# Kernel optimization log

Measured on AMD Instinct MI355X. Metric: run time of the kernel, lower is better.

Reference implementation:

```python
import jax, jax.numpy as jnp
import numpy as np

HEADS = 4

def _pair_msg(H, w2, B, xsrc):
    # H:[E,mid] radial-MLP hidden; w2:[mid,co,ci,nf]; B:[E,m_out,m_in,nf] CG/SH basis; xsrc:[E,ci,m_in]
    tmp = jnp.einsum('epqf,eiq->eipf', B, xsrc)          # basis-weighted input  [E,ci,m_out,nf]
    R = jnp.einsum('eh,hoif->eoif', H, w2)               # per-edge radial weights [E,co,ci,nf]
    return jnp.einsum('eoif,eipf->eop', R, tmp)          # edge message [E,co,m_out]

def _conv_edges(ef, w1, w2_nf1, w2_11, b00, b01, b10, b11, x0s, x1s):
    # pair index p = 2*d_in + d_out; pairs (0,0),(0,1),(1,0) have nf=1, pair (1,1) has nf=3
    H = jax.nn.relu(jnp.einsum('ef,pfh->peh', ef, w1))
    m0 = _pair_msg(H[0], w2_nf1[0][..., None], b00, x0s) + _pair_msg(H[2], w2_nf1[2][..., None], b10, x1s)
    m1 = _pair_msg(H[1], w2_nf1[1][..., None], b01, x0s) + _pair_msg(H[3], w2_11, b11, x1s)
    return m0, m1

def _seg_softmax(z, dst, n):
    m = jax.ops.segment_max(z, dst, num_segments=n)
    m = jnp.where(jnp.isfinite(m), m, 0.0)
    e = jnp.exp(z - m[dst])
    s = jax.ops.segment_sum(e, dst, num_segments=n)
    return e / (s[dst] + 1e-9)

def _norm_se3(x, g, b, eps=1e-3):
    n = jnp.sqrt((x * x).sum(-1) + 1e-12)                # per-channel irrep norm [N,C]
    mu = n.mean(-1, keepdims=True)
    var = ((n - mu) ** 2).mean(-1, keepdims=True)
    ln = (n - mu) / jnp.sqrt(var + 1e-5) * g + b
    return x * (jax.nn.relu(ln) / (n + eps))[..., None]

def _forward(x0, x1, edge_feat, b00, b01, b10, b11, kv_w1, kv_w2_nf1, kv_w2_11,
             wq, wproj, norm_gamma, norm_beta, fc_w1, fc_w2_nf1, fc_w2_11, fc_wself,
             edge_src, edge_dst):
    N = x0.shape[0]
    E = edge_src.shape[0]
    L = kv_w1.shape[0]
    ckv = wq.shape[-1]
    scale = 1.0 / np.sqrt((ckv // HEADS) * 4)            # key feats per head over degrees 0,1 (1+3 comps)
    hs = lambda t: t.reshape(t.shape[0], HEADS, ckv // HEADS, t.shape[-1])
    for l in range(L):
        # AttentionBlockSE3: ConvSE3 -> per-edge key/value; LinearSE3 -> query; seg-softmax attention
        kv0, kv1 = _conv_edges(edge_feat, kv_w1[l], kv_w2_nf1[l], kv_w2_11[l],
                               b00, b01, b10, b11, x0[edge_src], x1[edge_src])
        k0, v0 = kv0[:, :ckv], kv0[:, ckv:]
        k1, v1 = kv1[:, :ckv], kv1[:, ckv:]
        q0 = jnp.einsum('ncm,cd->ndm', x0, wq[l, 0])
        q1 = jnp.einsum('ncm,cd->ndm', x1, wq[l, 1])
        z = (hs(q0)[edge_dst] * hs(k0)).sum((2, 3)) + (hs(q1)[edge_dst] * hs(k1)).sum((2, 3))
        alpha = _seg_softmax(z * scale, edge_dst, N)     # [E,heads]
        a0 = (alpha[:, :, None, None] * hs(v0)).reshape(E, ckv, 1)
        a1 = (alpha[:, :, None, None] * hs(v1)).reshape(E, ckv, 3)
        o0 = jax.ops.segment_sum(a0, edge_dst, num_segments=N)
        o1 = jax.ops.segment_sum(a1, edge_dst, num_segments=N)
        # project concat(attn_out, skip) per degree, then NormSE3
        x0 = jnp.einsum('ncm,cd->ndm', jnp.concatenate([o0, x0], 1), wproj[l, 0])
        x1 = jnp.einsum('ncm,cd->ndm', jnp.concatenate([o1, x1], 1), wproj[l, 1])
        x0 = _norm_se3(x0, norm_gamma[l, 0], norm_beta[l, 0])
        x1 = _norm_se3(x1, norm_gamma[l, 1], norm_beta[l, 1])
    # final ConvSE3 with self-interaction, scatter-aggregated over dst nodes
    m0, m1 = _conv_edges(edge_feat, fc_w1, fc_w2_nf1, fc_w2_11,
                         b00, b01, b10, b11, x0[edge_src], x1[edge_src])
    y0 = jax.ops.segment_sum(m0, edge_dst, num_segments=N) + jnp.einsum('ncm,cd->ndm', x0, fc_wself[0])
    y1 = jax.ops.segment_sum(m1, edge_dst, num_segments=N) + jnp.einsum('ncm,cd->ndm', x1, fc_wself[1])
    return jnp.concatenate([y0.reshape(N, -1), y1.reshape(N, -1)], axis=1)

def setup_inputs() -> dict:
    key = jax.random.key(0)
    ks = jax.random.split(key, 20)
    N, E, C, L = 8192, 131072, 16, 2
    Fe, mid, KV, ckv, Co = 16, 16, 16, 8, 8
    f = lambda k, s, sc=1.0: jax.random.normal(k, s, dtype=jnp.float32) * sc
    return {
        'x0': f(ks[0], (N, C, 1)),
        'x1': f(ks[1], (N, C, 3)),
        'edge_feat': f(ks[2], (E, Fe)),
        'b00': f(ks[3], (E, 1, 1, 1)),
        'b01': f(ks[4], (E, 3, 1, 1)),
        'b10': f(ks[5], (E, 1, 3, 1)),
        'b11': f(ks[6], (E, 3, 3, 3)),
        'kv_w1': f(ks[7], (L, 4, Fe, mid), 0.1),
        'kv_w2_nf1': f(ks[8], (L, 3, mid, KV, C), 0.1),
        'kv_w2_11': f(ks[9], (L, mid, KV, C, 3), 0.1),
        'wq': f(ks[10], (L, 2, C, ckv), 0.1),
        'wproj': f(ks[11], (L, 2, ckv + C, C), 0.1),
        'norm_gamma': jnp.ones((L, 2, C), dtype=jnp.float32),
        'norm_beta': jnp.zeros((L, 2, C), dtype=jnp.float32),
        'fc_w1': f(ks[12], (4, Fe, mid), 0.1),
        'fc_w2_nf1': f(ks[13], (3, mid, Co, C), 0.1),
        'fc_w2_11': f(ks[14], (mid, Co, C, 3), 0.1),
        'fc_wself': f(ks[15], (2, C, Co), 0.1),
        'edge_src': jax.random.randint(ks[16], (E,), 0, N, dtype=jnp.int32),
        'edge_dst': jax.random.randint(ks[17], (E,), 0, N, dtype=jnp.int32),
    }

def reference(x0, x1, edge_feat, b00, b01, b10, b11, kv_w1, kv_w2_nf1, kv_w2_11,
              wq, wproj, norm_gamma, norm_beta, fc_w1, fc_w2_nf1, fc_w2_11, fc_wself,
              edge_src, edge_dst):
    return _forward(x0, x1, edge_feat, b00, b01, b10, b11, kv_w1, kv_w2_nf1, kv_w2_11,
                    wq, wproj, norm_gamma, norm_beta, fc_w1, fc_w2_nf1, fc_w2_11, fc_wself,
                    edge_src, edge_dst)
```

## Files before the change

kernel.cpp:

```cpp
#include <hip/hip_runtime.h>
#include <hip/hip_fp16.h>
#include <math.h>


typedef _Float16 half8 __attribute__((ext_vector_type(8)));
typedef float f32x4 __attribute__((ext_vector_type(4)));

union AF {
    half8 h8;
    __half2 h2[4];
};
union U32h2 {
    unsigned u;
    __half2 h;
};

__global__ void k_hist(const int* __restrict__ dst, int* __restrict__ counts, int E) {
    int e = blockIdx.x * 256 + threadIdx.x;
    if (e < E) atomicAdd(&counts[dst[e]], 1);
}

__global__ __launch_bounds__(1024) void k_scan(const int* __restrict__ counts,
                                               int* __restrict__ rowptr,
                                               int* __restrict__ cursor,
                                               int N, int CH) {
    __shared__ int part[1024];
    int t = threadIdx.x;
    int s = 0;
    for (int i = 0; i < CH; ++i) {
        int idx = t * CH + i;
        if (idx < N) s += counts[idx];
    }
    part[t] = s;
    __syncthreads();
    for (int off = 1; off < 1024; off <<= 1) {
        int v = (t >= off) ? part[t - off] : 0;
        __syncthreads();
        part[t] += v;
        __syncthreads();
    }
    int run = (t == 0) ? 0 : part[t - 1];
    for (int i = 0; i < CH; ++i) {
        int idx = t * CH + i;
        if (idx < N) {
            rowptr[idx] = run;
            cursor[idx] = run;
            run += counts[idx];
        }
    }
    if (t == 0) rowptr[N] = part[1023];
}

__global__ void k_scatter(const int* __restrict__ dst, int* __restrict__ cursor,
                          int* __restrict__ pose, int E) {
    int e = blockIdx.x * 256 + threadIdx.x;
    if (e < E) {
        int pos = atomicAdd(&cursor[dst[e]], 1);
        pose[e] = pos;
    }
}

__global__ void k_misc(const float* __restrict__ x0, const float* __restrict__ x1,
                       const float* __restrict__ ef,
                       float* __restrict__ xs0, float* __restrict__ xs1,
                       unsigned short* __restrict__ efh, int n0, int n1, int n2) {
    int i = blockIdx.x * 256 + threadIdx.x;
    if (i < n0) { xs0[i] = x0[i]; return; }
    i -= n0;
    if (i < n1) { xs1[i] = x1[i]; return; }
    i -= n1;
    if (i < n2) efh[i] = __half_as_ushort(__float2half(ef[i]));
}

__global__ void k_prepw(const float* __restrict__ kvw1, const float* __restrict__ fcw1,
                        const float* __restrict__ kvw2n, const float* __restrict__ kvw211,
                        const float* __restrict__ fcw2n, const float* __restrict__ fcw211,
                        unsigned short* __restrict__ Wfrag) {
    int t = blockIdx.x * 256 + threadIdx.x;
    if (t >= 156 * 64 * 8) return;
    int j = t & 7;
    int lane = (t >> 3) & 63;
    int row = t >> 9;
    int quad = lane >> 4, m = lane & 15;
    int c = row / 52, r = row % 52;
    int KVO = (c < 2) ? 16 : 8;
    const float* w1src = (c < 2) ? (kvw1 + c * 1024) : fcw1;
    const float* w2n = (c < 2) ? (kvw2n + c * 12288) : fcw2n;
    const float* w211 = (c < 2) ? (kvw211 + c * 12288) : fcw211;
    float v = 0.f;
    if (r < 4) {
        if (quad < 2) v = w1src[r * 256 + (quad * 8 + j) * 16 + m];
    } else if (r < 28) {
        int fam = (r - 4) >> 3, kk = (r - 4) & 7;
        int h = quad * 4 + ((j >> 1) & 3), i = 2 * kk + (j & 1);
        if (m < KVO) v = w2n[((fam * 16 + h) * KVO + m) * 16 + i];
    } else {
        int kk2 = r - 28;
        int h = quad * 4 + ((j >> 1) & 3);
        int ifx = 2 * kk2 + (j & 1);
        int i = ifx / 3, f = ifx % 3;
        if (m < KVO) v = w211[((h * KVO + m) * 16 + i) * 3 + f];
    }
    Wfrag[t] = __half_as_ushort(__float2half(v));
}

template <int KVO, bool DO_Z>
__global__ __launch_bounds__(256, 2) void k_conv(
    int E,
    const int* __restrict__ src, const int* __restrict__ dst,
    const int* __restrict__ pose,
    const float* __restrict__ xs0, const float* __restrict__ xs1,
    const float* __restrict__ b00, const float* __restrict__ b01,
    const float* __restrict__ b10, const float* __restrict__ b11,
    const unsigned short* __restrict__ efh,
    const unsigned short* __restrict__ Wfrag,
    int wbase,
    const float* __restrict__ q0, const float* __restrict__ q1,
    float* __restrict__ vrow, float* __restrict__ zb)
{
    __shared__ __align__(16) unsigned xBL[4][16 * 74];
    int tid = threadIdx.x;
    int wave = tid >> 6, lane = tid & 63;
    int tile = blockIdx.x * 4 + wave;
    if (tile * 16 >= E) return;
    int m = lane & 15, quad = lane >> 4;
    int e0 = tile * 16;
    int me = e0 + m;
    int s = src[me];
    unsigned* xw = xBL[wave];
    const half8* W8 = (const half8*)Wfrag;

    {
        float x1c[12];
        const float4* xp = (const float4*)(xs1 + (size_t)s * 48 + quad * 12);
#pragma unroll
        for (int cc = 0; cc < 3; ++cc) {
            float4 v = xp[cc];
            x1c[cc * 4 + 0] = v.x; x1c[cc * 4 + 1] = v.y;
            x1c[cc * 4 + 2] = v.z; x1c[cc * 4 + 3] = v.w;
        }
        float b11r[27];
#pragma unroll
        for (int k = 0; k < 27; ++k) b11r[k] = b11[(size_t)me * 27 + k];
#pragma unroll
        for (int p = 0; p < 3; ++p) {
            float vals[12];
#pragma unroll
            for (int i2 = 0; i2 < 4; ++i2) {
#pragma unroll
                for (int f = 0; f < 3; ++f) {
                    float a = 0.f;
#pragma unroll
                    for (int q = 0; q < 3; ++q) a += x1c[i2 * 3 + q] * b11r[p * 9 + q * 3 + f];
                    vals[i2 * 3 + f] = a;
                }
            }
            unsigned uu[6];
#pragma unroll
            for (int u = 0; u < 6; ++u) {
                U32h2 w;
                w.h = __float22half2_rn(make_float2(vals[2 * u], vals[2 * u + 1]));
                uu[u] = w.u;
            }
            int boff = m * 74 + p * 24 + quad * 6;
            *(uint2*)&xw[boff + 0] = make_uint2(uu[0], uu[1]);
            *(uint2*)&xw[boff + 2] = make_uint2(uu[2], uu[3]);
            *(uint2*)&xw[boff + 4] = make_uint2(uu[4], uu[5]);
        }
    }
    __syncthreads();

    __half2 x0p[8], t10p[8];
    {
        const float4* p = (const float4*)(xs0 + (size_t)s * 16);
#pragma unroll
        for (int k = 0; k < 4; ++k) {
            float4 v = p[k];
            x0p[2 * k + 0] = __float22half2_rn(make_float2(v.x, v.y));
            x0p[2 * k + 1] = __float22half2_rn(make_float2(v.z, v.w));
        }
        float bq0 = b10[(size_t)me * 3 + 0], bq1 = b10[(size_t)me * 3 + 1],
              bq2 = b10[(size_t)me * 3 + 2];
        const float4* xp = (const float4*)(xs1 + (size_t)s * 48);
        float tf[16];
#pragma unroll
        for (int g = 0; g < 4; ++g) {
            float4 a = xp[g * 3 + 0], b = xp[g * 3 + 1], cc = xp[g * 3 + 2];
            float xf[12] = {a.x, a.y, a.z, a.w, b.x, b.y, b.z, b.w, cc.x, cc.y, cc.z, cc.w};
#pragma unroll
            for (int i2 = 0; i2 < 4; ++i2)
                tf[g * 4 + i2] = bq0 * xf[i2 * 3] + bq1 * xf[i2 * 3 + 1] + bq2 * xf[i2 * 3 + 2];
        }
#pragma unroll
        for (int k = 0; k < 8; ++k)
            t10p[k] = __float22half2_rn(make_float2(tf[2 * k], tf[2 * k + 1]));
    }

    __half2 Hd[4][4];
    {
        half8 efr = {0, 0, 0, 0, 0, 0, 0, 0};
        if (quad < 2) efr = *(const half8*)(efh + (size_t)me * 16 + quad * 8);
        f32x4 z4 = {0.f, 0.f, 0.f, 0.f};
#pragma unroll
        for (int pp = 0; pp < 4; ++pp) {
            half8 w1f = W8[(size_t)(wbase + pp) * 64 + lane];
            f32x4 hacc = __builtin_amdgcn_mfma_f32_16x16x32_f16(w1f, efr, z4, 0, 0, 0);
#pragma unroll
            for (int r = 0; r < 4; ++r)
                Hd[pp][r] = __float2half2_rn(__float2half(fmaxf(hacc[r], 0.f)));
        }
    }

    f32x4 acc0 = {0.f, 0.f, 0.f, 0.f}, acc1 = acc0, acc2 = acc0;
    f32x4 accP0 = acc0, accP1 = acc0, accP2 = acc0;

#pragma unroll
    for (int kk = 0; kk < 8; ++kk) {
        __half2 xp_ = x0p[kk], tp_ = t10p[kk];
        AF a0, a1, a2;
#pragma unroll
        for (int t = 0; t < 4; ++t) {
            a0.h2[t] = __hmul2(Hd[0][t], xp_);
            a1.h2[t] = __hmul2(Hd[1][t], xp_);
            a2.h2[t] = __hmul2(Hd[2][t], tp_);
        }
        half8 w0 = W8[(size_t)(wbase + 4 + kk) * 64 + lane];
        half8 w1f = W8[(size_t)(wbase + 12 + kk) * 64 + lane];
        half8 w2f = W8[(size_t)(wbase + 20 + kk) * 64 + lane];
        acc0 = __builtin_amdgcn_mfma_f32_16x16x32_f16(w0, a0.h8, acc0, 0, 0, 0);
        acc1 = __builtin_amdgcn_mfma_f32_16x16x32_f16(w1f, a1.h8, acc1, 0, 0, 0);
        acc2 = __builtin_amdgcn_mfma_f32_16x16x32_f16(w2f, a2.h8, acc2, 0, 0, 0);
    }

#pragma unroll
    for (int kko = 0; kko < 12; ++kko) {
        uint2 xu0 = *(const uint2*)&xw[m * 74 + 0 * 24 + 2 * kko];
        uint2 xu1 = *(const uint2*)&xw[m * 74 + 1 * 24 + 2 * kko];
        uint2 xu2 = *(const uint2*)&xw[m * 74 + 2 * 24 + 2 * kko];
        unsigned pv0[2] = {xu0.x, xu0.y};
        unsigned pv1[2] = {xu1.x, xu1.y};
        unsigned pv2[2] = {xu2.x, xu2.y};
#pragma unroll
        for (int t = 0; t < 2; ++t) {
            U32h2 u0, u1, u2;
            u0.u = pv0[t]; u1.u = pv1[t]; u2.u = pv2[t];
            AF a0, a1, a2;
#pragma unroll
            for (int r = 0; r < 4; ++r) {
                a0.h2[r] = __hmul2(Hd[3][r], u0.h);
                a1.h2[r] = __hmul2(Hd[3][r], u1.h);
                a2.h2[r] = __hmul2(Hd[3][r], u2.h);
            }
            half8 wf = W8[(size_t)(wbase + 28 + 2 * kko + t) * 64 + lane];
            accP0 = __builtin_amdgcn_mfma_f32_16x16x32_f16(wf, a0.h8, accP0, 0, 0, 0);
            accP1 = __builtin_amdgcn_mfma_f32_16x16x32_f16(wf, a1.h8, accP1, 0, 0, 0);
            accP2 = __builtin_amdgcn_mfma_f32_16x16x32_f16(wf, a2.h8, accP2, 0, 0, 0);
        }
    }

    float b00r = b00[me];
    float b01r0 = b01[(size_t)me * 3 + 0], b01r1 = b01[(size_t)me * 3 + 1],
          b01r2 = b01[(size_t)me * 3 + 2];
    float o0v[4], o1v[4][3];
#pragma unroll
    for (int r = 0; r < 4; ++r) {
        o0v[r] = b00r * acc0[r] + acc2[r];
        o1v[r][0] = b01r0 * acc1[r] + accP0[r];
        o1v[r][1] = b01r1 * acc1[r] + accP1[r];
        o1v[r][2] = b01r2 * acc1[r] + accP2[r];
    }
    int pos = pose[me];
    bool doStore = DO_Z ? (quad >= 2) : (quad < 2);
    if (doStore) {
        int qa = DO_Z ? (quad - 2) : quad;
        float* vp = vrow + (size_t)pos * 32;
        *(float4*)&vp[qa * 4] = make_float4(o0v[0], o0v[1], o0v[2], o0v[3]);
        float* p1 = vp + 8 + qa * 12;
        *(float4*)&p1[0] = make_float4(o1v[0][0], o1v[0][1], o1v[0][2], o1v[1][0]);
        *(float4*)&p1[4] = make_float4(o1v[1][1], o1v[1][2], o1v[2][0], o1v[2][1]);
        *(float4*)&p1[8] = make_float4(o1v[2][2], o1v[3][0], o1v[3][1], o1v[3][2]);
    }
    if (DO_Z && quad < 2) {
        int n = dst[me];
        float4 q0v = *(const float4*)&q0[(size_t)n * 8 + quad * 4];
        const float4* q1p = (const float4*)&q1[(size_t)n * 24 + quad * 12];
        float4 qa4 = q1p[0], qb4 = q1p[1], qc4 = q1p[2];
        float q1f[12] = {qa4.x, qa4.y, qa4.z, qa4.w, qb4.x, qb4.y, qb4.z, qb4.w,
                         qc4.x, qc4.y, qc4.z, qc4.w};
        float q0f[4] = {q0v.x, q0v.y, q0v.z, q0v.w};
        float zh0 = 0.f, zh1 = 0.f;
#pragma unroll
        for (int r = 0; r < 4; ++r) {
            float tt = q0f[r] * o0v[r] + q1f[r * 3 + 0] * o1v[r][0] +
                       q1f[r * 3 + 1] * o1v[r][1] + q1f[r * 3 + 2] * o1v[r][2];
            if (r < 2) zh0 += tt;
            else zh1 += tt;
        }
        const float scale = 0.35355339059327373f;
        *(float2*)&zb[(size_t)pos * 4 + quad * 2] = make_float2(zh0 * scale, zh1 * scale);
    }
}

__global__ void k_q(int N, const float* __restrict__ xs0, const float* __restrict__ xs1,
                    const float* __restrict__ wq,
                    float* __restrict__ q0, float* __restrict__ q1) {
    int t = blockIdx.x * 256 + threadIdx.x;
    if (t >= N * 32) return;
    int n = t >> 5, comp = t & 31;
    if (comp < 8) {
        float a = 0.f;
#pragma unroll
        for (int c = 0; c < 16; ++c) a += xs0[n * 16 + c] * wq[c * 8 + comp];
        q0[n * 8 + comp] = a;
    } else {
        int idx = comp - 8, dd = idx / 3, mm = idx % 3;
        float a = 0.f;
#pragma unroll
        for (int c = 0; c < 16; ++c) a += xs1[n * 48 + c * 3 + mm] * wq[128 + c * 8 + dd];
        q1[n * 24 + dd * 3 + mm] = a;
    }
}

__global__ __launch_bounds__(256) void k_attn(
    int N,
    const int* __restrict__ rowptr,
    const float* __restrict__ zb, const float* __restrict__ vrow,
    const float* __restrict__ wproj,
    const float* __restrict__ gamma, const float* __restrict__ beta,
    float* __restrict__ xs0, float* __restrict__ xs1,
    const float* __restrict__ wq_next,
    float* __restrict__ q0, float* __restrict__ q1) {
    __shared__ float wpL[768];
    __shared__ float gL[32], btL[32];
    __shared__ float inb[16][100];
    __shared__ float aw[16][16][4];
    int tid = threadIdx.x;
    for (int i = tid; i < 768; i += 256) wpL[i] = wproj[i];
    if (tid < 32) { gL[tid] = gamma[tid]; btL[tid] = beta[tid]; }
    int wave = tid >> 6, lane = tid & 63;
    int sub = lane >> 4, l16 = lane & 15;
    int nodeIdx = wave * 4 + sub;
    int n = blockIdx.x * 16 + nodeIdx;
    if (n >= N) n = N - 1;
    int base = rowptr[n], deg = rowptr[n + 1] - base;
    const float4* zb4 = (const float4*)zb;

    float mx0 = -INFINITY, mx1 = -INFINITY, mx2 = -INFINITY, mx3 = -INFINITY;
    for (int j = l16; j < deg; j += 16) {
        float4 zv = zb4[base + j];
        mx0 = fmaxf(mx0, zv.x); mx1 = fmaxf(mx1, zv.y);
        mx2 = fmaxf(mx2, zv.z); mx3 = fmaxf(mx3, zv.w);
    }
#pragma unroll
    for (int off = 1; off < 16; off <<= 1) {
        mx0 = fmaxf(mx0, __shfl_xor(mx0, off));
        mx1 = fmaxf(mx1, __shfl_xor(mx1, off));
        mx2 = fmaxf(mx2, __shfl_xor(mx2, off));
        mx3 = fmaxf(mx3, __shfl_xor(mx3, off));
    }
    if (!isfinite(mx0)) mx0 = 0.f;
    if (!isfinite(mx1)) mx1 = 0.f;
    if (!isfinite(mx2)) mx2 = 0.f;
    if (!isfinite(mx3)) mx3 = 0.f;

    int c0 = 2 * l16, c1 = c0 + 1;
    int hA = ((c0 < 8) ? c0 : (c0 - 8) / 3) >> 1;
    int hB = ((c1 < 8) ? c1 : (c1 - 8) / 3) >> 1;
    float s0 = 0.f, s1 = 0.f, s2 = 0.f, s3 = 0.f;
    float accA = 0.f, accB = 0.f;
    for (int j0 = 0; j0 < deg; j0 += 16) {
        int j = j0 + l16;
        float4 a4 = make_float4(0.f, 0.f, 0.f, 0.f);
        if (j < deg) {
            float4 zv = zb4[base + j];
            a4.x = __expf(zv.x - mx0);
            a4.y = __expf(zv.y - mx1);
            a4.z = __expf(zv.z - mx2);
            a4.w = __expf(zv.w - mx3);
            s0 += a4.x; s1 += a4.y; s2 += a4.z; s3 += a4.w;
        }
        *(float4*)&aw[nodeIdx][l16][0] = a4;
        __builtin_amdgcn_wave_barrier();
        int cnt = min(16, deg - j0);
        const float* vbase = &vrow[(size_t)(base + j0) * 32 + c0];
        int jj = 0;
        for (; jj + 3 < cnt; jj += 4) {
            float2 v0 = *(const float2*)(vbase + (size_t)jj * 32);
            float2 v1 = *(const float2*)(vbase + (size_t)(jj + 1) * 32);
            float2 v2 = *(const float2*)(vbase + (size_t)(jj + 2) * 32);
            float2 v3 = *(const float2*)(vbase + (size_t)(jj + 3) * 32);
            accA += aw[nodeIdx][jj][hA] * v0.x + aw[nodeIdx][jj + 1][hA] * v1.x +
                    aw[nodeIdx][jj + 2][hA] * v2.x + aw[nodeIdx][jj + 3][hA] * v3.x;
            accB += aw[nodeIdx][jj][hB] * v0.y + aw[nodeIdx][jj + 1][hB] * v1.y +
                    aw[nodeIdx][jj + 2][hB] * v2.y + aw[nodeIdx][jj + 3][hB] * v3.y;
        }
        for (; jj < cnt; ++jj) {
            float2 v = *(const float2*)(vbase + (size_t)jj * 32);
            accA += aw[nodeIdx][jj][hA] * v.x;
            accB += aw[nodeIdx][jj][hB] * v.y;
        }
        __builtin_amdgcn_wave_barrier();
    }
#pragma unroll
    for (int off = 1; off < 16; off <<= 1) {
        s0 += __shfl_xor(s0, off); s1 += __shfl_xor(s1, off);
        s2 += __shfl_xor(s2, off); s3 += __shfl_xor(s3, off);
    }
    float inva[4] = {1.f / (s0 + 1e-9f), 1.f / (s1 + 1e-9f),
                     1.f / (s2 + 1e-9f), 1.f / (s3 + 1e-9f)};
    accA *= inva[hA];
    accB *= inva[hB];

    float* in0 = inb[nodeIdx];
    float* in1 = in0 + 24;
    if (c0 < 8) { in0[c0] = accA; in0[c1] = accB; }
    else        { in1[c0 - 8] = accA; in1[c1 - 8] = accB; }
    in0[8 + l16] = xs0[(size_t)n * 16 + l16];
    {
        const float* xp = xs1 + (size_t)n * 48 + l16 * 3;
        in1[24 + l16 * 3 + 0] = xp[0];
        in1[24 + l16 * 3 + 1] = xp[1];
        in1[24 + l16 * 3 + 2] = xp[2];
    }
    __syncthreads();

    int c = l16;
    float y0 = 0.f;
#pragma unroll
    for (int j = 0; j < 24; ++j) y0 += in0[j] * wpL[j * 16 + c];
    float y1v[3];
#pragma unroll
    for (int mm = 0; mm < 3; ++mm) {
        float y = 0.f;
#pragma unroll
        for (int j = 0; j < 24; ++j) y += in1[j * 3 + mm] * wpL[384 + j * 16 + c];
        y1v[mm] = y;
    }
    float n0 = sqrtf(y0 * y0 + 1e-12f);
    float n1 = sqrtf(y1v[0] * y1v[0] + y1v[1] * y1v[1] + y1v[2] * y1v[2] + 1e-12f);
    float mu0 = n0, mu1 = n1;
#pragma unroll
    for (int off = 1; off < 16; off <<= 1) {
        mu0 += __shfl_xor(mu0, off);
        mu1 += __shfl_xor(mu1, off);
    }
    mu0 *= 0.0625f; mu1 *= 0.0625f;
    float dv0 = n0 - mu0, dv1 = n1 - mu1;
    float var0 = dv0 * dv0, var1 = dv1 * dv1;
#pragma unroll
    for (int off = 1; off < 16; off <<= 1) {
        var0 += __shfl_xor(var0, off);
        var1 += __shfl_xor(var1, off);
    }
    var0 *= 0.0625f; var1 *= 0.0625f;
    float ln0 = dv0 * rsqrtf(var0 + 1e-5f) * gL[c] + btL[c];
    float ln1 = dv1 * rsqrtf(var1 + 1e-5f) * gL[16 + c] + btL[16 + c];
    float fac0 = fmaxf(ln0, 0.f) / (n0 + 1e-3f);
    float fac1 = fmaxf(ln1, 0.f) / (n1 + 1e-3f);
    float x0n = y0 * fac0;
    float x1n[3] = {y1v[0] * fac1, y1v[1] * fac1, y1v[2] * fac1};
    xs0[(size_t)n * 16 + c] = x0n;
    float* xo = xs1 + (size_t)n * 48 + c * 3;
    xo[0] = x1n[0]; xo[1] = x1n[1]; xo[2] = x1n[2];

    if (wq_next) {
        __builtin_amdgcn_wave_barrier();
        in0[8 + c] = x0n;
        in1[24 + c * 3 + 0] = x1n[0];
        in1[24 + c * 3 + 1] = x1n[1];
        in1[24 + c * 3 + 2] = x1n[2];
        __builtin_amdgcn_wave_barrier();
        int compA = 2 * l16, compB = compA + 1;
#pragma unroll
        for (int cb = 0; cb < 2; ++cb) {
            int comp = cb ? compB : compA;
            float a = 0.f;
            if (comp < 8) {
#pragma unroll
                for (int cc = 0; cc < 16; ++cc)
                    a += in0[8 + cc] * wq_next[cc * 8 + comp];
                q0[(size_t)n * 8 + comp] = a;
            } else {
                int idx = comp - 8, dd = idx / 3, mm = idx % 3;
#pragma unroll
                for (int cc = 0; cc < 16; ++cc)
                    a += in1[24 + cc * 3 + mm] * wq_next[128 + cc * 8 + dd];
                q1[(size_t)n * 24 + idx] = a;
            }
        }
    }
}

__global__ __launch_bounds__(256) void k_out(
    int N,
    const int* __restrict__ rowptr, const float* __restrict__ vrow,
    const float* __restrict__ xs0, const float* __restrict__ xs1,
    const float* __restrict__ wself,
    float* __restrict__ out) {
    int tid = threadIdx.x;
    int wave = tid >> 6, lane = tid & 63;
    int sub = lane >> 4, l16 = lane & 15;
    int n = blockIdx.x * 16 + wave * 4 + sub;
    if (n >= N) n = N - 1;
    int base = rowptr[n], deg = rowptr[n + 1] - base;

    int c0 = 2 * l16, c1 = c0 + 1;
    float accA = 0.f, accB = 0.f;
    const float* vbase = &vrow[(size_t)base * 32 + c0];
    int j = 0;
    for (; j + 3 < deg; j += 4) {
        float2 v0 = *(const float2*)(vbase + (size_t)j * 32);
        float2 v1 = *(const float2*)(vbase + (size_t)(j + 1) * 32);
        float2 v2 = *(const float2*)(vbase + (size_t)(j + 2) * 32);
        float2 v3 = *(const float2*)(vbase + (size_t)(j + 3) * 32);
        accA += v0.x + v1.x + v2.x + v3.x;
        accB += v0.y + v1.y + v2.y + v3.y;
    }
    for (; j < deg; ++j) {
        float2 v = *(const float2*)(vbase + (size_t)j * 32);
        accA += v.x;
        accB += v.y;
    }
    if (c0 < 8) {
#pragma unroll
        for (int c = 0; c < 16; ++c) {
            float xv = xs0[(size_t)n * 16 + c];
            accA += xv * wself[c * 8 + c0];
            accB += xv * wself[c * 8 + c1];
        }
    } else {
        int dA = (c0 - 8) / 3, mA = (c0 - 8) % 3;
        int dB = (c1 - 8) / 3, mB = (c1 - 8) % 3;
#pragma unroll
        for (int c = 0; c < 16; ++c) {
            accA += xs1[(size_t)n * 48 + c * 3 + mA] * wself[128 + c * 8 + dA];
            accB += xs1[(size_t)n * 48 + c * 3 + mB] * wself[128 + c * 8 + dB];
        }
    }
    *(float2*)&out[(size_t)n * 32 + c0] = make_float2(accA, accB);
}

extern "C" void kernel_launch(void* const* d_in, const int* in_sizes, int n_in,
                              void* d_out, int out_size, void* d_ws, size_t ws_size,
                              hipStream_t stream) {
    const float* x0 = (const float*)d_in[0];
    const float* x1 = (const float*)d_in[1];
    const float* ef = (const float*)d_in[2];
    const float* b00 = (const float*)d_in[3];
    const float* b01 = (const float*)d_in[4];
    const float* b10 = (const float*)d_in[5];
    const float* b11 = (const float*)d_in[6];
    const float* kvw1 = (const float*)d_in[7];
    const float* kvw2n = (const float*)d_in[8];
    const float* kvw211 = (const float*)d_in[9];
    const float* wq = (const float*)d_in[10];
    const float* wproj = (const float*)d_in[11];
    const float* gam = (const float*)d_in[12];
    const float* bet = (const float*)d_in[13];
    const float* fcw1 = (const float*)d_in[14];
    const float* fcw2n = (const float*)d_in[15];
    const float* fcw211 = (const float*)d_in[16];
    const float* fcself = (const float*)d_in[17];
    const int* esrc = (const int*)d_in[18];
    const int* edst = (const int*)d_in[19];
    int N = in_sizes[0] / 16;
    int E = in_sizes[18];
    float* out = (float*)d_out;

    float* ws = (float*)d_ws;
    size_t off = 0;
    float* xs0 = ws + off; off += (size_t)N * 16;
    float* xs1 = ws + off; off += (size_t)N * 48;
    float* q0b = ws + off; off += (size_t)N * 8;
    float* q1b = ws + off; off += (size_t)N * 24;
    float* vrow = ws + off; off += (size_t)E * 32;
    float* zb = ws + off; off += (size_t)E * 4;
    int* counts = (int*)(ws + off); off += N;
    int* rowptr = (int*)(ws + off); off += N + 1;
    int* cursor = (int*)(ws + off); off += N;
    int* pose = (int*)(ws + off); off += E;
    off = (off + 3) & ~(size_t)3;
    unsigned short* efh = (unsigned short*)(ws + off); off += (size_t)E * 16 / 2;
    unsigned short* Wfrag = (unsigned short*)(ws + off); off += (size_t)156 * 64 * 8 / 2;

    const int tpb = 256;
    int ebl = (E + 255) / 256;
    int cblk = (E / 16 + 3) / 4;
    int nbl16 = (N + 15) / 16;

    k_prepw<<<(156 * 512 + 255) / 256, tpb, 0, stream>>>(kvw1, fcw1, kvw2n, kvw211,
                                                         fcw2n, fcw211, Wfrag);
    int mtot = N * 64 + E * 16;
    k_misc<<<(mtot + 255) / 256, tpb, 0, stream>>>(x0, x1, ef, xs0, xs1, efh,
                                                   N * 16, N * 48, E * 16);
    hipMemsetAsync(counts, 0, (size_t)N * 4, stream);
    k_hist<<<ebl, tpb, 0, stream>>>(edst, counts, E);
    int CH = (N + 1023) / 1024;
    k_scan<<<1, 1024, 0, stream>>>(counts, rowptr, cursor, N, CH);
    k_scatter<<<ebl, tpb, 0, stream>>>(edst, cursor, pose, E);
    k_q<<<(N * 32 + 255) / 256, tpb, 0, stream>>>(N, xs0, xs1, wq, q0b, q1b);

    k_conv<16, true><<<cblk, tpb, 0, stream>>>(E, esrc, edst, pose, xs0, xs1,
                                               b00, b01, b10, b11, efh, Wfrag, 0,
                                               q0b, q1b, vrow, zb);
    k_attn<<<nbl16, tpb, 0, stream>>>(N, rowptr, zb, vrow, wproj,
                                      gam, bet, xs0, xs1, wq + 256, q0b, q1b);
    k_conv<16, true><<<cblk, tpb, 0, stream>>>(E, esrc, edst, pose, xs0, xs1,
                                               b00, b01, b10, b11, efh, Wfrag, 52,
                                               q0b, q1b, vrow, zb);
    k_attn<<<nbl16, tpb, 0, stream>>>(N, rowptr, zb, vrow, wproj + 768,
                                      gam + 32, bet + 32, xs0, xs1, nullptr, q0b, q1b);
    k_conv<8, false><<<cblk, tpb, 0, stream>>>(E, esrc, edst, pose, xs0, xs1,
                                               b00, b01, b10, b11, efh, Wfrag, 104,
                                               q0b, q1b, vrow, zb);
    k_out<<<nbl16, tpb, 0, stream>>>(N, rowptr, vrow, xs0, xs1, fcself, out);
}
```

Before: 300.0 us.

## Merge setup kernels and stage b11 basis through shared memory in conv

Folds the weight-fragment prep, input copies, edge-feature conversion and initial query projection into one init kernel, which removes two launches. In the conv kernel, each wave now loads its tile's b11 basis rows cooperatively into padded shared memory with coalesced reads. Before, each lane read 27 strided floats straight from global memory. It also drops the min-blocks-per-CU hint from launch_bounds. The trade-off is extra LDS use plus a block-wide barrier, and the register and occupancy balance may shift.

```diff
diff --git a/kernel.cpp b/kernel.cpp
--- a/kernel.cpp
+++ b/kernel.cpp
@@ -60,52 +60,72 @@
     }
 }
 
-__global__ void k_misc(const float* __restrict__ x0, const float* __restrict__ x1,
+__global__ void k_init(const float* __restrict__ x0, const float* __restrict__ x1,
                        const float* __restrict__ ef,
+                       const float* __restrict__ kvw1, const float* __restrict__ fcw1,
+                       const float* __restrict__ kvw2n, const float* __restrict__ kvw211,
+                       const float* __restrict__ fcw2n, const float* __restrict__ fcw211,
+                       const float* __restrict__ wq,
                        float* __restrict__ xs0, float* __restrict__ xs1,
-                       unsigned short* __restrict__ efh, int n0, int n1, int n2) {
+                       unsigned short* __restrict__ efh,
+                       unsigned short* __restrict__ Wfrag,
+                       float* __restrict__ q0, float* __restrict__ q1,
+                       int N, int E) {
     int i = blockIdx.x * 256 + threadIdx.x;
-    if (i < n0) { xs0[i] = x0[i]; return; }
-    i -= n0;
-    if (i < n1) { xs1[i] = x1[i]; return; }
-    i -= n1;
-    if (i < n2) efh[i] = __half_as_ushort(__float2half(ef[i]));
-}
-
-__global__ void k_prepw(const float* __restrict__ kvw1, const float* __restrict__ fcw1,
-                        const float* __restrict__ kvw2n, const float* __restrict__ kvw211,
-                        const float* __restrict__ fcw2n, const float* __restrict__ fcw211,
-                        unsigned short* __restrict__ Wfrag) {
-    int t = blockIdx.x * 256 + threadIdx.x;
-    if (t >= 156 * 64 * 8) return;
-    int j = t & 7;
-    int lane = (t >> 3) & 63;
-    int row = t >> 9;
-    int quad = lane >> 4, m = lane & 15;
-    int c = row / 52, r = row % 52;
-    int KVO = (c < 2) ? 16 : 8;
-    const float* w1src = (c < 2) ? (kvw1 + c * 1024) : fcw1;
-    const float* w2n = (c < 2) ? (kvw2n + c * 12288) : fcw2n;
-    const float* w211 = (c < 2) ? (kvw211 + c * 12288) : fcw211;
-    float v = 0.f;
-    if (r < 4) {
-        if (quad < 2) v = w1src[r * 256 + (quad * 8 + j) * 16 + m];
-    } else if (r < 28) {
-        int fam = (r - 4) >> 3, kk = (r - 4) & 7;
-        int h = quad * 4 + ((j >> 1) & 3), i = 2 * kk + (j & 1);
-        if (m < KVO) v = w2n[((fam * 16 + h) * KVO + m) * 16 + i];
-    } else {
-        int kk2 = r - 28;
-        int h = quad * 4 + ((j >> 1) & 3);
-        int ifx = 2 * kk2 + (j & 1);
-        int i = ifx / 3, f = ifx % 3;
-        if (m < KVO) v = w211[((h * KVO + m) * 16 + i) * 3 + f];
-    }
-    Wfrag[t] = __half_as_ushort(__float2half(v));
+    if (i < 156 * 64 * 8) {
+        int t = i;
+        int j = t & 7;
+        int lane = (t >> 3) & 63;
+        int row = t >> 9;
+        int quad = lane >> 4, m = lane & 15;
+        int c = row / 52, r = row % 52;
+        int KVO = (c < 2) ? 16 : 8;
+        const float* w1src = (c < 2) ? (kvw1 + c * 1024) : fcw1;
+        const float* w2n = (c < 2) ? (kvw2n + c * 12288) : fcw2n;
+        const float* w211 = (c < 2) ? (kvw211 + c * 12288) : fcw211;
+        float v = 0.f;
+        if (r < 4) {
+            if (quad < 2) v = w1src[r * 256 + (quad * 8 + j) * 16 + m];
+        } else if (r < 28) {
+            int fam = (r - 4) >> 3, kk = (r - 4) & 7;
+            int h = quad * 4 + ((j >> 1) & 3), ii = 2 * kk + (j & 1);
+            if (m < KVO) v = w2n[((fam * 16 + h) * KVO + m) * 16 + ii];
+        } else {
+            int kk2 = r - 28;
+            int h = quad * 4 + ((j >> 1) & 3);
+            int ifx = 2 * kk2 + (j & 1);
+            int ii = ifx / 3, f = ifx % 3;
+            if (m < KVO) v = w211[((h * KVO + m) * 16 + ii) * 3 + f];
+        }
+        Wfrag[t] = __half_as_ushort(__float2half(v));
+        return;
+    }
+    i -= 156 * 64 * 8;
+    if (i < N * 16) { xs0[i] = x0[i]; return; }
+    i -= N * 16;
+    if (i < N * 48) { xs1[i] = x1[i]; return; }
+    i -= N * 48;
+    if (i < E * 16) { efh[i] = __half_as_ushort(__float2half(ef[i])); return; }
+    i -= E * 16;
+    if (i < N * 32) {
+        int n = i >> 5, comp = i & 31;
+        if (comp < 8) {
+            float a = 0.f;
+#pragma unroll
+            for (int c = 0; c < 16; ++c) a += x0[n * 16 + c] * wq[c * 8 + comp];
+            q0[n * 8 + comp] = a;
+        } else {
+            int idx = comp - 8, dd = idx / 3, mm = idx % 3;
+            float a = 0.f;
+#pragma unroll
+            for (int c = 0; c < 16; ++c) a += x1[n * 48 + c * 3 + mm] * wq[128 + c * 8 + dd];
+            q1[n * 24 + dd * 3 + mm] = a;
+        }
+    }
 }
 
 template <int KVO, bool DO_Z>
-__global__ __launch_bounds__(256, 2) void k_conv(
+__global__ __launch_bounds__(256) void k_conv(
     int E,
     const int* __restrict__ src, const int* __restrict__ dst,
     const int* __restrict__ pose,
@@ -119,6 +139,7 @@
     float* __restrict__ vrow, float* __restrict__ zb)
 {
     __shared__ __align__(16) unsigned xBL[4][16 * 74];
+    __shared__ float b11L[4][16 * 29];
     int tid = threadIdx.x;
     int wave = tid >> 6, lane = tid & 63;
     int tile = blockIdx.x * 4 + wave;
@@ -131,6 +152,20 @@
     const half8* W8 = (const half8*)Wfrag;
 
     {
+        const float* gb = b11 + (size_t)e0 * 27;
+        float* lb = b11L[wave];
+#pragma unroll
+        for (int it = 0; it < 7; ++it) {
+            int d = it * 64 + lane;
+            if (d < 432) {
+                int ee = d / 27, kk = d - ee * 27;
+                lb[ee * 29 + kk] = gb[d];
+            }
+        }
+    }
+    __syncthreads();
+
+    {
         float x1c[12];
         const float4* xp = (const float4*)(xs1 + (size_t)s * 48 + quad * 12);
 #pragma unroll
@@ -139,9 +174,10 @@
             x1c[cc * 4 + 0] = v.x; x1c[cc * 4 + 1] = v.y;
             x1c[cc * 4 + 2] = v.z; x1c[cc * 4 + 3] = v.w;
         }
+        const float* lb = &b11L[wave][m * 29];
         float b11r[27];
 #pragma unroll
-        for (int k = 0; k < 27; ++k) b11r[k] = b11[(size_t)me * 27 + k];
+        for (int k = 0; k < 27; ++k) b11r[k] = lb[k];
 #pragma unroll
         for (int p = 0; p < 3; ++p) {
             float vals[12];
@@ -298,26 +334,6 @@
         }
         const float scale = 0.35355339059327373f;
         *(float2*)&zb[(size_t)pos * 4 + quad * 2] = make_float2(zh0 * scale, zh1 * scale);
-    }
-}
-
-__global__ void k_q(int N, const float* __restrict__ xs0, const float* __restrict__ xs1,
-                    const float* __restrict__ wq,
-                    float* __restrict__ q0, float* __restrict__ q1) {
-    int t = blockIdx.x * 256 + threadIdx.x;
-    if (t >= N * 32) return;
-    int n = t >> 5, comp = t & 31;
-    if (comp < 8) {
-        float a = 0.f;
-#pragma unroll
-        for (int c = 0; c < 16; ++c) a += xs0[n * 16 + c] * wq[c * 8 + comp];
-        q0[n * 8 + comp] = a;
-    } else {
-        int idx = comp - 8, dd = idx / 3, mm = idx % 3;
-        float a = 0.f;
-#pragma unroll
-        for (int c = 0; c < 16; ++c) a += xs1[n * 48 + c * 3 + mm] * wq[128 + c * 8 + dd];
-        q1[n * 24 + dd * 3 + mm] = a;
     }
 }
 
@@ -588,17 +604,15 @@
     int cblk = (E / 16 + 3) / 4;
     int nbl16 = (N + 15) / 16;
 
-    k_prepw<<<(156 * 512 + 255) / 256, tpb, 0, stream>>>(kvw1, fcw1, kvw2n, kvw211,
-                                                         fcw2n, fcw211, Wfrag);
-    int mtot = N * 64 + E * 16;
-    k_misc<<<(mtot + 255) / 256, tpb, 0, stream>>>(x0, x1, ef, xs0, xs1, efh,
-                                                   N * 16, N * 48, E * 16);
+    int itot = 156 * 512 + N * 16 + N * 48 + E * 16 + N * 32;
+    k_init<<<(itot + 255) / 256, tpb, 0, stream>>>(x0, x1, ef, kvw1, fcw1, kvw2n, kvw211,
+                                                   fcw2n, fcw211, wq, xs0, xs1, efh,
+                                                   Wfrag, q0b, q1b, N, E);
     hipMemsetAsync(counts, 0, (size_t)N * 4, stream);
     k_hist<<<ebl, tpb, 0, stream>>>(edst, counts, E);
     int CH = (N + 1023) / 1024;
     k_scan<<<1, 1024, 0, stream>>>(counts, rowptr, cursor, N, CH);
     k_scatter<<<ebl, tpb, 0, stream>>>(edst, cursor, pose, E);
-    k_q<<<(N * 32 + 255) / 256, tpb, 0, stream>>>(N, xs0, xs1, wq, q0b, q1b);
 
     k_conv<16, true><<<cblk, tpb, 0, stream>>>(E, esrc, edst, pose, xs0, xs1,
                                                b00, b01, b10, b11, efh, Wfrag, 0,
```

New measurement: 299.0 us. About the same (-0.3%).
